# Optimization experiments

Hardware: AMD Instinct MI355X
Metric: run time of the kernel (lower is better)

## Reference

```python
import jax, jax.numpy as jnp
import numpy as np

B_, S, D_IN, D_OUT, N_ADP, R = 4, 4096, 2048, 2048, 4, 16
SCALE = 32.0 / 16.0  # lora_alpha / r, use_rslora=False, same for all adaptors


def setup_inputs() -> dict:
    key = jax.random.key(0)
    ks = jax.random.split(key, 6)
    x = jax.random.normal(ks[0], (B_, S, D_IN), dtype=jnp.float32)
    mask = jax.random.uniform(ks[1], (N_ADP, B_, S, 1), dtype=jnp.float32)
    W = jax.random.normal(ks[2], (D_OUT, D_IN), dtype=jnp.float32) * 0.02
    b = jnp.zeros((D_OUT,), dtype=jnp.float32)
    A = jax.random.normal(ks[3], (N_ADP, R, D_IN), dtype=jnp.float32) * 0.02
    Bw = jax.random.normal(ks[4], (N_ADP, D_OUT, R), dtype=jnp.float32) * 0.02
    return {"x": x, "mask": mask, "W": W, "b": b, "A": A, "Bw": Bw}


def reference(x, mask, W, b, A, Bw):
    # base_layer: y = x @ W^T + b  -> [B, S, D_OUT]
    result = jnp.einsum('bsd,od->bso', x, W) + b
    # all adaptors batched: h = lora_A(x) -> [N, B, S, R]
    h = jnp.einsum('bsd,nrd->nbsr', x, A)
    # delta = lora_B(h) -> [N, B, S, D_OUT]
    delta = jnp.einsum('nbsr,nor->nbso', h, Bw)
    # scale, per-adaptor mask multiply, accumulate into residual
    result = result + jnp.sum(delta * SCALE * mask, axis=0)
    return result
```

## Files before the change

kernel.cpp:

```cpp
#include <hip/hip_runtime.h>
#include <stdint.h>


typedef __attribute__((ext_vector_type(8))) short bf16x8;
typedef __attribute__((ext_vector_type(4))) float f32x4;
typedef __attribute__((ext_vector_type(4))) unsigned short u16x4;
typedef __attribute__((ext_vector_type(8))) unsigned short u16x8;

#define GAS __attribute__((address_space(1)))
#define LAS __attribute__((address_space(3)))

static constexpr int BB   = 4;
static constexpr int SS   = 4096;
static constexpr int DIN  = 2048;
static constexpr int DOUT = 2048;
static constexpr int NADP = 4;
static constexpr int RR   = 16;
static constexpr int M    = BB * SS;
static constexpr int KA   = DIN + NADP * RR;
static constexpr float SCALE = 2.0f;

static constexpr int KSPLIT = 4;
static constexpr int KCH    = DIN / KSPLIT;

static_assert(KA % 64 == 0, "K-loop needs BK=64 divisibility");

__device__ __forceinline__ unsigned short f2bf(float f) {
  union { float f; uint32_t u; } v; v.f = f;
  uint32_t u = v.u;
  return (unsigned short)((u + 0x7FFFu + ((u >> 16) & 1u)) >> 16);
}

__global__ __launch_bounds__(256) void pass1a_conv_hpart(
    const float* __restrict__ x, const float* __restrict__ A,
    unsigned short* __restrict__ Xaug, float* __restrict__ Hpart)
{
  __shared__ unsigned short xb[64 * 64];
  __shared__ unsigned short ab[64 * 64];

  const int tid = threadIdx.x;
  const int rb = blockIdx.x >> 2;
  const int ks = blockIdx.x & 3;
  const int rowBase = rb * 64;
  const int kBase = ks * KCH;
  const int w = tid >> 6, lane = tid & 63;
  const int quad = lane >> 4, m16 = lane & 15;

  f32x4 acc[4];
  #pragma unroll
  for (int j = 0; j < 4; ++j) acc[j] = f32x4{0.f, 0.f, 0.f, 0.f};

  for (int kc = kBase; kc < kBase + KCH; kc += 64) {
    __syncthreads();
    #pragma unroll
    for (int l = 0; l < 4; ++l) {
      int v = l * 256 + tid;
      int r = v >> 4;
      int k = (v & 15) * 4;
      float4 xv = *(const float4*)(x + (size_t)(rowBase + r) * DIN + kc + k);
      u16x4 xq = { f2bf(xv.x), f2bf(xv.y), f2bf(xv.z), f2bf(xv.w) };
      *(u16x4*)(xb + r * 64 + k) = xq;
      *(u16x4*)(Xaug + (size_t)(rowBase + r) * KA + kc + k) = xq;
      float4 av = *(const float4*)(A + (size_t)r * DIN + kc + k);
      u16x4 aq = { f2bf(av.x), f2bf(av.y), f2bf(av.z), f2bf(av.w) };
      *(u16x4*)(ab + r * 64 + k) = aq;
    }
    __syncthreads();
    #pragma unroll
    for (int s = 0; s < 2; ++s) {
      bf16x8 af = *(const bf16x8*)(xb + (w * 16 + m16) * 64 + s * 32 + quad * 8);
      #pragma unroll
      for (int jt = 0; jt < 4; ++jt) {
        bf16x8 bfg = *(const bf16x8*)(ab + (jt * 16 + m16) * 64 + s * 32 + quad * 8);
        acc[jt] = __builtin_amdgcn_mfma_f32_16x16x32_bf16(af, bfg, acc[jt], 0, 0, 0);
      }
    }
  }

  const int grow0 = rowBase + w * 16 + quad * 4;
  #pragma unroll
  for (int jt = 0; jt < 4; ++jt) {
    #pragma unroll
    for (int r = 0; r < 4; ++r) {
      int grow = grow0 + r;
      Hpart[(((size_t)ks * M + grow) << 6) + jt * 16 + m16] = acc[jt][r];
    }
  }
}

__global__ __launch_bounds__(256) void pass1b_reduce_mask(
    const float* __restrict__ Hpart, const float* __restrict__ mask,
    unsigned short* __restrict__ Xaug)
{
  const int idx = blockIdx.x * 256 + threadIdx.x;
  const int row = idx >> 6;
  const int j   = idx & 63;
  float s = 0.f;
  #pragma unroll
  for (int ks = 0; ks < KSPLIT; ++ks)
    s += Hpart[(((size_t)ks * M) << 6) + idx];
  s *= mask[(size_t)(j >> 4) * M + row];
  Xaug[(size_t)row * KA + DIN + j] = f2bf(s);
}

__global__ __launch_bounds__(256) void pass2_wcvt(
    const float* __restrict__ W, const float* __restrict__ Bw,
    unsigned short* __restrict__ Waug)
{
  const int idx = blockIdx.x * 256 + threadIdx.x;
  const int row = idx >> 8;
  const int k   = (idx & 255) * 8;
  float4 a = *(const float4*)(W + (size_t)row * DIN + k);
  float4 b = *(const float4*)(W + (size_t)row * DIN + k + 4);
  u16x8 q = { f2bf(a.x), f2bf(a.y), f2bf(a.z), f2bf(a.w),
              f2bf(b.x), f2bf(b.y), f2bf(b.z), f2bf(b.w) };
  *(u16x8*)(Waug + (size_t)row * KA + k) = q;

  if (idx < DOUT * NADP) {
    const int col = idx >> 2, n = idx & 3;
    const float* src = Bw + (size_t)n * DOUT * RR + (size_t)col * RR;
    #pragma unroll
    for (int t = 0; t < 4; ++t) {
      float4 bv = *(const float4*)(src + 4 * t);
      u16x4 qq = { f2bf(SCALE * bv.x), f2bf(SCALE * bv.y),
                   f2bf(SCALE * bv.z), f2bf(SCALE * bv.w) };
      *(u16x4*)(Waug + (size_t)col * KA + DIN + n * 16 + 4 * t) = qq;
    }
  }
}

__global__ __launch_bounds__(256, 3) void gemm_aug(
    const unsigned short* __restrict__ Xa, const unsigned short* __restrict__ Wa,
    const float* __restrict__ bias, float* __restrict__ out)
{
  __shared__ unsigned short lds_a[128 * 64];
  __shared__ unsigned short lds_b[128 * 64];

  const int tid = threadIdx.x;
  const int bn = blockIdx.x, bm = blockIdx.y;
  const int w = tid >> 6, lane = tid & 63;
  const int wm = w >> 1, wn = w & 1;
  const int quad = lane >> 4, m16 = lane & 15;

  f32x4 acc[4][4];
  #pragma unroll
  for (int i = 0; i < 4; ++i)
    #pragma unroll
    for (int j = 0; j < 4; ++j) acc[i][j] = f32x4{0.f, 0.f, 0.f, 0.f};

  const unsigned short* ga = Xa + (size_t)bm * 128 * KA;
  const unsigned short* gb = Wa + (size_t)bn * 128 * KA;

  size_t goff[4];
  int ldso[4];
  #pragma unroll
  for (int l = 0; l < 4; ++l) {
    int p = l * 256 + tid;
    int r = p >> 3;
    int c = (p & 7) ^ (r & 7);
    goff[l] = (size_t)r * KA + c * 8;
    ldso[l] = (l * 256 + (tid & ~63)) * 8;
  }

  for (int k0 = 0; k0 < KA; k0 += 64) {
    __syncthreads();
    #pragma unroll
    for (int l = 0; l < 4; ++l) {
      __builtin_amdgcn_global_load_lds((const GAS void*)(ga + goff[l] + k0),
                                       (LAS void*)(lds_a + ldso[l]), 16, 0, 0);
      __builtin_amdgcn_global_load_lds((const GAS void*)(gb + goff[l] + k0),
                                       (LAS void*)(lds_b + ldso[l]), 16, 0, 0);
    }
    __syncthreads();

    #pragma unroll
    for (int s = 0; s < 2; ++s) {
      const int cc = ((s * 4 + quad) ^ (m16 & 7)) * 8;
      bf16x8 af[4], bfg[4];
      #pragma unroll
      for (int i = 0; i < 4; ++i)
        af[i] = *(const bf16x8*)(lds_a + (wm * 64 + i * 16 + m16) * 64 + cc);
      #pragma unroll
      for (int j = 0; j < 4; ++j)
        bfg[j] = *(const bf16x8*)(lds_b + (wn * 64 + j * 16 + m16) * 64 + cc);
      #pragma unroll
      for (int i = 0; i < 4; ++i)
        #pragma unroll
        for (int j = 0; j < 4; ++j)
          acc[i][j] = __builtin_amdgcn_mfma_f32_16x16x32_bf16(af[i], bfg[j],
                                                              acc[i][j], 0, 0, 0);
    }
  }

  float bv[4];
  #pragma unroll
  for (int j = 0; j < 4; ++j) bv[j] = bias[bn * 128 + wn * 64 + j * 16 + m16];
  #pragma unroll
  for (int i = 0; i < 4; ++i) {
    const int row0 = bm * 128 + wm * 64 + i * 16 + quad * 4;
    #pragma unroll
    for (int j = 0; j < 4; ++j) {
      const int col = bn * 128 + wn * 64 + j * 16 + m16;
      #pragma unroll
      for (int r = 0; r < 4; ++r)
        out[(size_t)(row0 + r) * DOUT + col] = acc[i][j][r] + bv[j];
    }
  }
}

extern "C" void kernel_launch(void* const* d_in, const int* in_sizes, int n_in,
                              void* d_out, int out_size, void* d_ws, size_t ws_size,
                              hipStream_t stream) {
  const float* x    = (const float*)d_in[0];
  const float* mask = (const float*)d_in[1];
  const float* W    = (const float*)d_in[2];
  const float* bias = (const float*)d_in[3];
  const float* A    = (const float*)d_in[4];
  const float* Bw   = (const float*)d_in[5];
  float* out = (float*)d_out;

  unsigned short* Xaug = (unsigned short*)d_ws;
  unsigned short* Waug = Xaug + (size_t)M * KA;
  float* Hpart = (float*)(Waug + (size_t)DOUT * KA);

  pass1a_conv_hpart<<<dim3(M / 64 * KSPLIT), dim3(256), 0, stream>>>(x, A, Xaug, Hpart);
  pass1b_reduce_mask<<<dim3(M * 64 / 256), dim3(256), 0, stream>>>(Hpart, mask, Xaug);
  pass2_wcvt<<<dim3((DOUT * (DIN / 8)) / 256), dim3(256), 0, stream>>>(W, Bw, Waug);
  gemm_aug<<<dim3(DOUT / 128, M / 128), dim3(256), 0, stream>>>(Xaug, Waug, bias, out);
}
```

Measured before the change: 401.7 us.

## Triple-buffer GEMM K-loop with 256x128 tiles, 512 threads and XCD-aware block swizzle

After: 465.9 us. 16.0% more time.

```diff
diff --git a/kernel.cpp b/kernel.cpp
--- a/kernel.cpp
+++ b/kernel.cpp
@@ -22,6 +22,10 @@
 
 static constexpr int KSPLIT = 4;
 static constexpr int KCH    = DIN / KSPLIT;
+
+static constexpr int NT    = KA / 64;
+static constexpr int ASLOT = 256 * 64;
+static constexpr int BSLOT = 128 * 64;
 
 static_assert(KA % 64 == 0, "K-loop needs BK=64 divisibility");
 
@@ -129,15 +133,31 @@
   }
 }
 
-__global__ __launch_bounds__(256, 3) void gemm_aug(
+__device__ __forceinline__ void stage_tile(
+    const unsigned short* __restrict__ ga, const unsigned short* __restrict__ gb,
+    unsigned short* sa, unsigned short* sb, int k0,
+    const int* goa, const int* loa, const int* gob, const int* lob)
+{
+  #pragma unroll
+  for (int l = 0; l < 4; ++l)
+    __builtin_amdgcn_global_load_lds((const GAS void*)(ga + goa[l] + k0),
+                                     (LAS void*)(sa + loa[l]), 16, 0, 0);
+  #pragma unroll
+  for (int l = 0; l < 2; ++l)
+    __builtin_amdgcn_global_load_lds((const GAS void*)(gb + gob[l] + k0),
+                                     (LAS void*)(sb + lob[l]), 16, 0, 0);
+}
+
+__global__ __launch_bounds__(512, 2) void gemm_aug(
     const unsigned short* __restrict__ Xa, const unsigned short* __restrict__ Wa,
     const float* __restrict__ bias, float* __restrict__ out)
 {
-  __shared__ unsigned short lds_a[128 * 64];
-  __shared__ unsigned short lds_b[128 * 64];
+  __shared__ unsigned short lds_a[3 * ASLOT];
+  __shared__ unsigned short lds_b[3 * BSLOT];
 
   const int tid = threadIdx.x;
-  const int bn = blockIdx.x, bm = blockIdx.y;
+  const int lin = ((int)blockIdx.x & 7) * 128 + ((int)blockIdx.x >> 3);
+  const int bn = lin & 15, bm = lin >> 4;
   const int w = tid >> 6, lane = tid & 63;
   const int wm = w >> 1, wn = w & 1;
   const int quad = lane >> 4, m16 = lane & 15;
@@ -148,48 +168,67 @@
     #pragma unroll
     for (int j = 0; j < 4; ++j) acc[i][j] = f32x4{0.f, 0.f, 0.f, 0.f};
 
-  const unsigned short* ga = Xa + (size_t)bm * 128 * KA;
+  const unsigned short* ga = Xa + (size_t)bm * 256 * KA;
   const unsigned short* gb = Wa + (size_t)bn * 128 * KA;
 
-  size_t goff[4];
-  int ldso[4];
+  int goa[4], loa[4], gob[2], lob[2];
   #pragma unroll
   for (int l = 0; l < 4; ++l) {
-    int p = l * 256 + tid;
+    int p = l * 512 + tid;
     int r = p >> 3;
     int c = (p & 7) ^ (r & 7);
-    goff[l] = (size_t)r * KA + c * 8;
-    ldso[l] = (l * 256 + (tid & ~63)) * 8;
-  }
-
-  for (int k0 = 0; k0 < KA; k0 += 64) {
-    __syncthreads();
-    #pragma unroll
-    for (int l = 0; l < 4; ++l) {
-      __builtin_amdgcn_global_load_lds((const GAS void*)(ga + goff[l] + k0),
-                                       (LAS void*)(lds_a + ldso[l]), 16, 0, 0);
-      __builtin_amdgcn_global_load_lds((const GAS void*)(gb + goff[l] + k0),
-                                       (LAS void*)(lds_b + ldso[l]), 16, 0, 0);
-    }
-    __syncthreads();
-
+    goa[l] = r * KA + c * 8;
+    loa[l] = (l * 512 + (tid & ~63)) * 8;
+  }
+  #pragma unroll
+  for (int l = 0; l < 2; ++l) {
+    int p = l * 512 + tid;
+    int r = p >> 3;
+    int c = (p & 7) ^ (r & 7);
+    gob[l] = r * KA + c * 8;
+    lob[l] = (l * 512 + (tid & ~63)) * 8;
+  }
+
+  stage_tile(ga, gb, lds_a, lds_b, 0, goa, loa, gob, lob);
+  stage_tile(ga, gb, lds_a + ASLOT, lds_b + BSLOT, 64, goa, loa, gob, lob);
+  asm volatile("s_waitcnt vmcnt(6)" ::: "memory");
+  __builtin_amdgcn_s_barrier();
+  __builtin_amdgcn_sched_barrier(0);
+
+  int cs = 0;
+  for (int t = 0; t < NT; ++t) {
+    int ss = cs + 2; if (ss >= 3) ss -= 3;
+    if (t + 2 < NT)
+      stage_tile(ga, gb, lds_a + ss * ASLOT, lds_b + ss * BSLOT, (t + 2) * 64,
+                 goa, loa, gob, lob);
+
+    const unsigned short* sa = lds_a + cs * ASLOT;
+    const unsigned short* sb = lds_b + cs * BSLOT;
     #pragma unroll
     for (int s = 0; s < 2; ++s) {
       const int cc = ((s * 4 + quad) ^ (m16 & 7)) * 8;
       bf16x8 af[4], bfg[4];
       #pragma unroll
       for (int i = 0; i < 4; ++i)
-        af[i] = *(const bf16x8*)(lds_a + (wm * 64 + i * 16 + m16) * 64 + cc);
+        af[i] = *(const bf16x8*)(sa + (wm * 64 + i * 16 + m16) * 64 + cc);
       #pragma unroll
       for (int j = 0; j < 4; ++j)
-        bfg[j] = *(const bf16x8*)(lds_b + (wn * 64 + j * 16 + m16) * 64 + cc);
+        bfg[j] = *(const bf16x8*)(sb + (wn * 64 + j * 16 + m16) * 64 + cc);
+      __builtin_amdgcn_s_setprio(1);
       #pragma unroll
       for (int i = 0; i < 4; ++i)
         #pragma unroll
         for (int j = 0; j < 4; ++j)
           acc[i][j] = __builtin_amdgcn_mfma_f32_16x16x32_bf16(af[i], bfg[j],
                                                               acc[i][j], 0, 0, 0);
-    }
+      __builtin_amdgcn_s_setprio(0);
+    }
+
+    if (t + 2 < NT) asm volatile("s_waitcnt vmcnt(6)" ::: "memory");
+    else            asm volatile("s_waitcnt vmcnt(0)" ::: "memory");
+    __builtin_amdgcn_s_barrier();
+    __builtin_amdgcn_sched_barrier(0);
+    cs += 1; if (cs >= 3) cs -= 3;
   }
 
   float bv[4];
@@ -197,7 +236,7 @@
   for (int j = 0; j < 4; ++j) bv[j] = bias[bn * 128 + wn * 64 + j * 16 + m16];
   #pragma unroll
   for (int i = 0; i < 4; ++i) {
-    const int row0 = bm * 128 + wm * 64 + i * 16 + quad * 4;
+    const int row0 = bm * 256 + wm * 64 + i * 16 + quad * 4;
     #pragma unroll
     for (int j = 0; j < 4; ++j) {
       const int col = bn * 128 + wn * 64 + j * 16 + m16;
@@ -226,5 +265,5 @@
   pass1a_conv_hpart<<<dim3(M / 64 * KSPLIT), dim3(256), 0, stream>>>(x, A, Xaug, Hpart);
   pass1b_reduce_mask<<<dim3(M * 64 / 256), dim3(256), 0, stream>>>(Hpart, mask, Xaug);
   pass2_wcvt<<<dim3((DOUT * (DIN / 8)) / 256), dim3(256), 0, stream>>>(W, Bw, Waug);
-  gemm_aug<<<dim3(DOUT / 128, M / 128), dim3(256), 0, stream>>>(Xaug, Waug, bias, out);
-}
+  gemm_aug<<<dim3(1024), dim3(512), 0, stream>>>(Xaug, Waug, bias, out);
+}
```

## Rewrite augmented GEMM as 256x256 tile, 8-wave, double-buffered half-K pipeline

Applied to the files above, without the earlier changes.

Result: slower. 456.5 us (+13.6%).

```diff
diff --git a/kernel.cpp b/kernel.cpp
--- a/kernel.cpp
+++ b/kernel.cpp
@@ -23,7 +23,11 @@
 static constexpr int KSPLIT = 4;
 static constexpr int KCH    = DIN / KSPLIT;
 
+static constexpr int NT  = KA / 64;
+static constexpr int HTS = 256 * 32;
+
 static_assert(KA % 64 == 0, "K-loop needs BK=64 divisibility");
+static_assert(NT >= 3, "tail specialization assumes >=3 K-steps");
 
 __device__ __forceinline__ unsigned short f2bf(float f) {
   union { float f; uint32_t u; } v; v.f = f;
@@ -129,78 +133,160 @@
   }
 }
 
-__global__ __launch_bounds__(256, 3) void gemm_aug(
+struct Stg { int so0, so1, do0, do1; };
+
+__device__ __forceinline__ void phase_barrier() {
+  __builtin_amdgcn_sched_barrier(0);
+  __builtin_amdgcn_s_barrier();
+  __builtin_amdgcn_sched_barrier(0);
+}
+
+__device__ __forceinline__ void stage_half(
+    const unsigned short* __restrict__ g, unsigned short* l, int koff,
+    const Stg& s)
+{
+  __builtin_amdgcn_global_load_lds((const GAS void*)(g + s.so0 + koff),
+                                   (LAS void*)(l + s.do0), 16, 0, 0);
+  __builtin_amdgcn_global_load_lds((const GAS void*)(g + s.so1 + koff),
+                                   (LAS void*)(l + s.do1), 16, 0, 0);
+}
+
+template<int VM1, int VM3, bool S0, bool S1, bool S2, bool S3>
+__device__ __forceinline__ void kstep(int t,
+    const unsigned short* __restrict__ ga, const unsigned short* __restrict__ gb,
+    unsigned short* la, unsigned short* lb, const Stg& st,
+    int rowA, int rowB, f32x4 (&acc)[8][4])
+{
+  const int cb = (t & 1) * (2 * HTS);
+  const int nb = cb ^ (2 * HTS);
+  const unsigned short* A0 = la + cb;
+  const unsigned short* B0 = lb + cb;
+  const unsigned short* A1 = A0 + HTS;
+  const unsigned short* B1 = B0 + HTS;
+  bf16x8 af[4], bfg[4];
+
+  if (S0) stage_half(gb, lb + nb, (t + 1) * 64, st);
+  #pragma unroll
+  for (int j = 0; j < 4; ++j) bfg[j] = *(const bf16x8*)(B0 + rowB + j * 512);
+  #pragma unroll
+  for (int ii = 0; ii < 4; ++ii) af[ii] = *(const bf16x8*)(A0 + rowA + ii * 512);
+  __builtin_amdgcn_s_setprio(1);
+  #pragma unroll
+  for (int ii = 0; ii < 4; ++ii)
+    #pragma unroll
+    for (int j = 0; j < 4; ++j)
+      acc[ii][j] = __builtin_amdgcn_mfma_f32_16x16x32_bf16(af[ii], bfg[j],
+                                                           acc[ii][j], 0, 0, 0);
+  __builtin_amdgcn_s_setprio(0);
+  phase_barrier();
+
+  if (S1) stage_half(ga, la + nb + HTS, (t + 1) * 64 + 32, st);
+  #pragma unroll
+  for (int ii = 0; ii < 4; ++ii)
+    af[ii] = *(const bf16x8*)(A0 + rowA + 2048 + ii * 512);
+  __builtin_amdgcn_s_setprio(1);
+  #pragma unroll
+  for (int ii = 0; ii < 4; ++ii)
+    #pragma unroll
+    for (int j = 0; j < 4; ++j)
+      acc[4 + ii][j] = __builtin_amdgcn_mfma_f32_16x16x32_bf16(af[ii], bfg[j],
+                                                               acc[4 + ii][j], 0, 0, 0);
+  __builtin_amdgcn_s_setprio(0);
+  if constexpr (VM1 >= 0)
+    asm volatile("s_waitcnt vmcnt(%0)" :: "i"(VM1) : "memory");
+  phase_barrier();
+
+  if (S2) stage_half(gb, lb + nb + HTS, (t + 1) * 64 + 32, st);
+  #pragma unroll
+  for (int j = 0; j < 4; ++j) bfg[j] = *(const bf16x8*)(B1 + rowB + j * 512);
+  #pragma unroll
+  for (int ii = 0; ii < 4; ++ii) af[ii] = *(const bf16x8*)(A1 + rowA + ii * 512);
+  __builtin_amdgcn_s_setprio(1);
+  #pragma unroll
+  for (int ii = 0; ii < 4; ++ii)
+    #pragma unroll
+    for (int j = 0; j < 4; ++j)
+      acc[ii][j] = __builtin_amdgcn_mfma_f32_16x16x32_bf16(af[ii], bfg[j],
+                                                           acc[ii][j], 0, 0, 0);
+  __builtin_amdgcn_s_setprio(0);
+  phase_barrier();
+
+  if (S3) stage_half(ga, la + cb, (t + 2) * 64, st);
+  #pragma unroll
+  for (int ii = 0; ii < 4; ++ii)
+    af[ii] = *(const bf16x8*)(A1 + rowA + 2048 + ii * 512);
+  __builtin_amdgcn_s_setprio(1);
+  #pragma unroll
+  for (int ii = 0; ii < 4; ++ii)
+    #pragma unroll
+    for (int j = 0; j < 4; ++j)
+      acc[4 + ii][j] = __builtin_amdgcn_mfma_f32_16x16x32_bf16(af[ii], bfg[j],
+                                                               acc[4 + ii][j], 0, 0, 0);
+  __builtin_amdgcn_s_setprio(0);
+  if constexpr (VM3 >= 0)
+    asm volatile("s_waitcnt vmcnt(%0)" :: "i"(VM3) : "memory");
+  phase_barrier();
+}
+
+__global__ __launch_bounds__(512, 2) void gemm_aug(
     const unsigned short* __restrict__ Xa, const unsigned short* __restrict__ Wa,
     const float* __restrict__ bias, float* __restrict__ out)
 {
-  __shared__ unsigned short lds_a[128 * 64];
-  __shared__ unsigned short lds_b[128 * 64];
+  __shared__ unsigned short lds_a[4 * HTS];
+  __shared__ unsigned short lds_b[4 * HTS];
 
   const int tid = threadIdx.x;
-  const int bn = blockIdx.x, bm = blockIdx.y;
+  const int lin = ((int)blockIdx.x & 7) * 64 + ((int)blockIdx.x >> 3);
+  const int bm = lin >> 3, bn = lin & 7;
   const int w = tid >> 6, lane = tid & 63;
-  const int wm = w >> 1, wn = w & 1;
+  const int wm = w >> 2, wn = w & 3;
   const int quad = lane >> 4, m16 = lane & 15;
 
-  f32x4 acc[4][4];
-  #pragma unroll
-  for (int i = 0; i < 4; ++i)
+  f32x4 acc[8][4];
+  #pragma unroll
+  for (int i = 0; i < 8; ++i)
     #pragma unroll
     for (int j = 0; j < 4; ++j) acc[i][j] = f32x4{0.f, 0.f, 0.f, 0.f};
 
-  const unsigned short* ga = Xa + (size_t)bm * 128 * KA;
-  const unsigned short* gb = Wa + (size_t)bn * 128 * KA;
-
-  size_t goff[4];
-  int ldso[4];
-  #pragma unroll
-  for (int l = 0; l < 4; ++l) {
-    int p = l * 256 + tid;
-    int r = p >> 3;
-    int c = (p & 7) ^ (r & 7);
-    goff[l] = (size_t)r * KA + c * 8;
-    ldso[l] = (l * 256 + (tid & ~63)) * 8;
-  }
-
-  for (int k0 = 0; k0 < KA; k0 += 64) {
-    __syncthreads();
-    #pragma unroll
-    for (int l = 0; l < 4; ++l) {
-      __builtin_amdgcn_global_load_lds((const GAS void*)(ga + goff[l] + k0),
-                                       (LAS void*)(lds_a + ldso[l]), 16, 0, 0);
-      __builtin_amdgcn_global_load_lds((const GAS void*)(gb + goff[l] + k0),
-                                       (LAS void*)(lds_b + ldso[l]), 16, 0, 0);
-    }
-    __syncthreads();
-
-    #pragma unroll
-    for (int s = 0; s < 2; ++s) {
-      const int cc = ((s * 4 + quad) ^ (m16 & 7)) * 8;
-      bf16x8 af[4], bfg[4];
-      #pragma unroll
-      for (int i = 0; i < 4; ++i)
-        af[i] = *(const bf16x8*)(lds_a + (wm * 64 + i * 16 + m16) * 64 + cc);
-      #pragma unroll
-      for (int j = 0; j < 4; ++j)
-        bfg[j] = *(const bf16x8*)(lds_b + (wn * 64 + j * 16 + m16) * 64 + cc);
-      #pragma unroll
-      for (int i = 0; i < 4; ++i)
-        #pragma unroll
-        for (int j = 0; j < 4; ++j)
-          acc[i][j] = __builtin_amdgcn_mfma_f32_16x16x32_bf16(af[i], bfg[j],
-                                                              acc[i][j], 0, 0, 0);
-    }
-  }
+  const unsigned short* ga = Xa + (size_t)bm * 256 * KA;
+  const unsigned short* gb = Wa + (size_t)bn * 256 * KA;
+
+  Stg st;
+  {
+    int p0 = tid, r0 = p0 >> 2, c0 = (p0 & 3) ^ (r0 & 3);
+    int p1 = 512 + tid, r1 = p1 >> 2, c1 = (p1 & 3) ^ (r1 & 3);
+    st.so0 = r0 * KA + c0 * 8;
+    st.so1 = r1 * KA + c1 * 8;
+    st.do0 = (tid & ~63) * 8;
+    st.do1 = (512 + (tid & ~63)) * 8;
+  }
+
+  const int cswz = (quad ^ (m16 & 3)) * 8;
+  const int rowA = (wm * 128 + m16) * 32 + cswz;
+  const int rowB = (wn * 64 + m16) * 32 + cswz;
+
+  stage_half(ga, lds_a, 0, st);
+  stage_half(gb, lds_b, 0, st);
+  stage_half(ga, lds_a + HTS, 32, st);
+  stage_half(gb, lds_b + HTS, 32, st);
+  stage_half(ga, lds_a + 2 * HTS, 64, st);
+  asm volatile("s_waitcnt vmcnt(6)" ::: "memory");
+  phase_barrier();
+
+  for (int t = 0; t < NT - 2; ++t)
+    kstep<6, 6, true, true, true, true>(t, ga, gb, lds_a, lds_b, st, rowA, rowB, acc);
+  kstep<6, 4, true, true, true, false>(NT - 2, ga, gb, lds_a, lds_b, st, rowA, rowB, acc);
+  kstep<0, -1, false, false, false, false>(NT - 1, ga, gb, lds_a, lds_b, st, rowA, rowB, acc);
 
   float bv[4];
   #pragma unroll
-  for (int j = 0; j < 4; ++j) bv[j] = bias[bn * 128 + wn * 64 + j * 16 + m16];
-  #pragma unroll
-  for (int i = 0; i < 4; ++i) {
-    const int row0 = bm * 128 + wm * 64 + i * 16 + quad * 4;
+  for (int j = 0; j < 4; ++j) bv[j] = bias[bn * 256 + wn * 64 + j * 16 + m16];
+  #pragma unroll
+  for (int i = 0; i < 8; ++i) {
+    const int row0 = bm * 256 + wm * 128 + i * 16 + quad * 4;
     #pragma unroll
     for (int j = 0; j < 4; ++j) {
-      const int col = bn * 128 + wn * 64 + j * 16 + m16;
+      const int col = bn * 256 + wn * 64 + j * 16 + m16;
       #pragma unroll
       for (int r = 0; r < 4; ++r)
         out[(size_t)(row0 + r) * DOUT + col] = acc[i][j][r] + bv[j];
@@ -226,5 +312,5 @@
   pass1a_conv_hpart<<<dim3(M / 64 * KSPLIT), dim3(256), 0, stream>>>(x, A, Xaug, Hpart);
   pass1b_reduce_mask<<<dim3(M * 64 / 256), dim3(256), 0, stream>>>(Hpart, mask, Xaug);
   pass2_wcvt<<<dim3((DOUT * (DIN / 8)) / 256), dim3(256), 0, stream>>>(W, Bw, Waug);
-  gemm_aug<<<dim3(DOUT / 128, M / 128), dim3(256), 0, stream>>>(Xaug, Waug, bias, out);
-}
+  gemm_aug<<<dim3(512), dim3(512), 0, stream>>>(Xaug, Waug, bias, out);
+}
```

## Rewrite main GEMM as 256x256 tiled, double-buffered LDS pipeline with 8 waves

Applied to the files above, without the earlier changes.

New measurement: 428.3 us. 6.6% more time.

```diff
diff --git a/kernel.cpp b/kernel.cpp
--- a/kernel.cpp
+++ b/kernel.cpp
@@ -23,7 +23,11 @@
 static constexpr int KSPLIT = 4;
 static constexpr int KCH    = DIN / KSPLIT;
 
+static constexpr int NT = KA / 64;
+static constexpr int HT = 128 * 64;
+
 static_assert(KA % 64 == 0, "K-loop needs BK=64 divisibility");
+static_assert(NT >= 2, "pipeline needs >=2 K-steps");
 
 __device__ __forceinline__ unsigned short f2bf(float f) {
   union { float f; uint32_t u; } v; v.f = f;
@@ -129,81 +133,152 @@
   }
 }
 
-__global__ __launch_bounds__(256, 3) void gemm_aug(
+struct Stg { int so, dofs; };
+
+__device__ __forceinline__ void gate_barrier() {
+  __builtin_amdgcn_sched_barrier(0);
+  __builtin_amdgcn_s_barrier();
+  __builtin_amdgcn_sched_barrier(0);
+}
+
+__device__ __forceinline__ void stage_half(
+    const unsigned short* __restrict__ g, unsigned short* l, int koff,
+    const Stg& st)
+{
+  __builtin_amdgcn_global_load_lds((const GAS void*)(g + st.so + koff),
+                                   (LAS void*)(l + st.dofs), 16, 0, 0);
+  __builtin_amdgcn_global_load_lds((const GAS void*)(g + st.so + 64 * KA + koff),
+                                   (LAS void*)(l + st.dofs + 4096), 16, 0, 0);
+}
+
+template<int VM1, int VM3, bool S>
+__device__ __forceinline__ void kstep(int t,
+    const unsigned short* __restrict__ ga, const unsigned short* __restrict__ gb,
+    unsigned short* la, unsigned short* lb, const Stg& st,
+    int rowA, int rowB, const int (&cc)[2], f32x4 (&acc)[8][4])
+{
+  const int cp = (t & 1) * (2 * HT);
+  const int np = cp ^ (2 * HT);
+  const unsigned short* A0 = la + cp;
+  const unsigned short* A1 = la + cp + HT;
+  const unsigned short* B0 = lb + cp;
+  const unsigned short* B1 = lb + cp + HT;
+  bf16x8 af[4][2], bA[2][2], bB[2][2];
+
+  if (S) {
+    stage_half(ga, la + np, (t + 1) * 64, st);
+    stage_half(gb, lb + np, (t + 1) * 64, st);
+    stage_half(gb + 128 * KA, lb + np + HT, (t + 1) * 64, st);
+  }
+  #pragma unroll
+  for (int i = 0; i < 4; ++i)
+    #pragma unroll
+    for (int kk = 0; kk < 2; ++kk)
+      af[i][kk] = *(const bf16x8*)(A0 + rowA + i * 1024 + cc[kk]);
+  #pragma unroll
+  for (int j = 0; j < 2; ++j)
+    #pragma unroll
+    for (int kk = 0; kk < 2; ++kk) {
+      bA[j][kk] = *(const bf16x8*)(B0 + rowB + j * 1024 + cc[kk]);
+      bB[j][kk] = *(const bf16x8*)(B1 + rowB + j * 1024 + cc[kk]);
+    }
+  __builtin_amdgcn_s_setprio(1);
+  #pragma unroll
+  for (int kk = 0; kk < 2; ++kk)
+    #pragma unroll
+    for (int i = 0; i < 4; ++i)
+      #pragma unroll
+      for (int j = 0; j < 2; ++j) {
+        acc[i][j]     = __builtin_amdgcn_mfma_f32_16x16x32_bf16(af[i][kk], bA[j][kk], acc[i][j], 0, 0, 0);
+        acc[i][2 + j] = __builtin_amdgcn_mfma_f32_16x16x32_bf16(af[i][kk], bB[j][kk], acc[i][2 + j], 0, 0, 0);
+      }
+  __builtin_amdgcn_s_setprio(0);
+  asm volatile("s_waitcnt vmcnt(%0)" :: "i"(VM1) : "memory");
+  gate_barrier();
+
+  if (S) stage_half(ga + 128 * KA, la + np + HT, (t + 1) * 64, st);
+  #pragma unroll
+  for (int i = 0; i < 4; ++i)
+    #pragma unroll
+    for (int kk = 0; kk < 2; ++kk)
+      af[i][kk] = *(const bf16x8*)(A1 + rowA + i * 1024 + cc[kk]);
+  __builtin_amdgcn_s_setprio(1);
+  #pragma unroll
+  for (int kk = 0; kk < 2; ++kk)
+    #pragma unroll
+    for (int i = 0; i < 4; ++i)
+      #pragma unroll
+      for (int j = 0; j < 2; ++j) {
+        acc[4 + i][j]     = __builtin_amdgcn_mfma_f32_16x16x32_bf16(af[i][kk], bA[j][kk], acc[4 + i][j], 0, 0, 0);
+        acc[4 + i][2 + j] = __builtin_amdgcn_mfma_f32_16x16x32_bf16(af[i][kk], bB[j][kk], acc[4 + i][2 + j], 0, 0, 0);
+      }
+  __builtin_amdgcn_s_setprio(0);
+  if constexpr (VM3 >= 0) {
+    asm volatile("s_waitcnt vmcnt(%0)" :: "i"(VM3) : "memory");
+    gate_barrier();
+  }
+}
+
+__global__ __launch_bounds__(512, 2) void gemm_aug(
     const unsigned short* __restrict__ Xa, const unsigned short* __restrict__ Wa,
     const float* __restrict__ bias, float* __restrict__ out)
 {
-  __shared__ unsigned short lds_a[128 * 64];
-  __shared__ unsigned short lds_b[128 * 64];
+  __shared__ unsigned short lds_a[4 * HT];
+  __shared__ unsigned short lds_b[4 * HT];
 
   const int tid = threadIdx.x;
-  const int bn = blockIdx.x, bm = blockIdx.y;
+  const int lin = ((int)blockIdx.x & 7) * 64 + ((int)blockIdx.x >> 3);
+  const int bm = lin >> 3, bn = lin & 7;
   const int w = tid >> 6, lane = tid & 63;
-  const int wm = w >> 1, wn = w & 1;
+  const int wm = w >> 2, wn = w & 3;
   const int quad = lane >> 4, m16 = lane & 15;
 
-  f32x4 acc[4][4];
-  #pragma unroll
-  for (int i = 0; i < 4; ++i)
+  f32x4 acc[8][4];
+  #pragma unroll
+  for (int i = 0; i < 8; ++i)
     #pragma unroll
     for (int j = 0; j < 4; ++j) acc[i][j] = f32x4{0.f, 0.f, 0.f, 0.f};
 
-  const unsigned short* ga = Xa + (size_t)bm * 128 * KA;
-  const unsigned short* gb = Wa + (size_t)bn * 128 * KA;
-
-  size_t goff[4];
-  int ldso[4];
-  #pragma unroll
-  for (int l = 0; l < 4; ++l) {
-    int p = l * 256 + tid;
-    int r = p >> 3;
-    int c = (p & 7) ^ (r & 7);
-    goff[l] = (size_t)r * KA + c * 8;
-    ldso[l] = (l * 256 + (tid & ~63)) * 8;
-  }
-
-  for (int k0 = 0; k0 < KA; k0 += 64) {
-    __syncthreads();
-    #pragma unroll
-    for (int l = 0; l < 4; ++l) {
-      __builtin_amdgcn_global_load_lds((const GAS void*)(ga + goff[l] + k0),
-                                       (LAS void*)(lds_a + ldso[l]), 16, 0, 0);
-      __builtin_amdgcn_global_load_lds((const GAS void*)(gb + goff[l] + k0),
-                                       (LAS void*)(lds_b + ldso[l]), 16, 0, 0);
-    }
-    __syncthreads();
-
-    #pragma unroll
-    for (int s = 0; s < 2; ++s) {
-      const int cc = ((s * 4 + quad) ^ (m16 & 7)) * 8;
-      bf16x8 af[4], bfg[4];
-      #pragma unroll
-      for (int i = 0; i < 4; ++i)
-        af[i] = *(const bf16x8*)(lds_a + (wm * 64 + i * 16 + m16) * 64 + cc);
-      #pragma unroll
-      for (int j = 0; j < 4; ++j)
-        bfg[j] = *(const bf16x8*)(lds_b + (wn * 64 + j * 16 + m16) * 64 + cc);
-      #pragma unroll
-      for (int i = 0; i < 4; ++i)
-        #pragma unroll
-        for (int j = 0; j < 4; ++j)
-          acc[i][j] = __builtin_amdgcn_mfma_f32_16x16x32_bf16(af[i], bfg[j],
-                                                              acc[i][j], 0, 0, 0);
-    }
-  }
+  const unsigned short* ga = Xa + (size_t)bm * 256 * KA;
+  const unsigned short* gb = Wa + (size_t)bn * 256 * KA;
+
+  Stg st;
+  {
+    int r = tid >> 3, c = (tid & 7) ^ (r & 7);
+    st.so   = r * KA + c * 8;
+    st.dofs = (tid & ~63) * 8;
+  }
+
+  int cc[2];
+  cc[0] = (quad ^ (m16 & 7)) * 8;
+  cc[1] = ((4 + quad) ^ (m16 & 7)) * 8;
+  const int rowA = (wm * 64 + m16) * 64;
+  const int rowB = (wn * 32 + m16) * 64;
+
+  stage_half(ga, lds_a, 0, st);
+  stage_half(gb, lds_b, 0, st);
+  stage_half(gb + 128 * KA, lds_b + HT, 0, st);
+  stage_half(ga + 128 * KA, lds_a + HT, 0, st);
+  asm volatile("s_waitcnt vmcnt(2)" ::: "memory");
+  gate_barrier();
+
+  for (int t = 0; t < NT - 1; ++t)
+    kstep<6, 2, true>(t, ga, gb, lds_a, lds_b, st, rowA, rowB, cc, acc);
+  kstep<0, -1, false>(NT - 1, ga, gb, lds_a, lds_b, st, rowA, rowB, cc, acc);
 
   float bv[4];
   #pragma unroll
-  for (int j = 0; j < 4; ++j) bv[j] = bias[bn * 128 + wn * 64 + j * 16 + m16];
-  #pragma unroll
-  for (int i = 0; i < 4; ++i) {
-    const int row0 = bm * 128 + wm * 64 + i * 16 + quad * 4;
-    #pragma unroll
-    for (int j = 0; j < 4; ++j) {
-      const int col = bn * 128 + wn * 64 + j * 16 + m16;
+  for (int jj = 0; jj < 4; ++jj)
+    bv[jj] = bias[bn * 256 + (jj >> 1) * 128 + wn * 32 + (jj & 1) * 16 + m16];
+  #pragma unroll
+  for (int I = 0; I < 8; ++I) {
+    const int row0 = bm * 256 + (I >> 2) * 128 + wm * 64 + (I & 3) * 16 + quad * 4;
+    #pragma unroll
+    for (int jj = 0; jj < 4; ++jj) {
+      const int col = bn * 256 + (jj >> 1) * 128 + wn * 32 + (jj & 1) * 16 + m16;
       #pragma unroll
       for (int r = 0; r < 4; ++r)
-        out[(size_t)(row0 + r) * DOUT + col] = acc[i][j][r] + bv[j];
+        out[(size_t)(row0 + r) * DOUT + col] = acc[I][jj][r] + bv[jj];
     }
   }
 }
@@ -226,5 +301,5 @@
   pass1a_conv_hpart<<<dim3(M / 64 * KSPLIT), dim3(256), 0, stream>>>(x, A, Xaug, Hpart);
   pass1b_reduce_mask<<<dim3(M * 64 / 256), dim3(256), 0, stream>>>(Hpart, mask, Xaug);
   pass2_wcvt<<<dim3((DOUT * (DIN / 8)) / 256), dim3(256), 0, stream>>>(W, Bw, Waug);
-  gemm_aug<<<dim3(DOUT / 128, M / 128), dim3(256), 0, stream>>>(Xaug, Waug, bias, out);
-}
+  gemm_aug<<<dim3(512), dim3(512), 0, stream>>>(Xaug, Waug, bias, out);
+}
```
